# Kernel optimization log

Measured on AMD Instinct MI355X. Metric: run time of the kernel, lower is better.

## Reference

```python
import jax, jax.numpy as jnp
import numpy as np

CH = 256
CQK = CH // 8
B, H, W = 4, 64, 64


def setup_inputs() -> dict:
    key = jax.random.key(0)
    ks = jax.random.split(key, 8)
    s_qk = 1.0 / np.sqrt(CH)  # MSR init for 1x1 conv: std = 1/sqrt(fan_in)
    x = jax.random.normal(ks[0], (B, CH, H, W), dtype=jnp.float32)
    Wq = jax.random.normal(ks[1], (CQK, CH), dtype=jnp.float32) * s_qk
    bq = jnp.zeros((CQK,), dtype=jnp.float32)
    Wk = jax.random.normal(ks[2], (CQK, CH), dtype=jnp.float32) * s_qk
    bk = jnp.zeros((CQK,), dtype=jnp.float32)
    Wv = jax.random.normal(ks[3], (CH, CH), dtype=jnp.float32) * s_qk
    bv = jnp.zeros((CH,), dtype=jnp.float32)
    # NOTE: module inits gamma=0; use a nonzero value so the attention branch is active
    gamma = jnp.float32(0.5) * jnp.ones((1,), dtype=jnp.float32)
    return {"x": x, "Wq": Wq, "bq": bq, "Wk": Wk, "bk": bk, "Wv": Wv, "bv": bv, "gamma": gamma}


def reference(x, Wq, bq, Wk, bk, Wv, bv, gamma):
    b, c, h, w = x.shape
    n = h * w
    xf = x.reshape(b, c, n)  # [B, C, N]
    # 1x1 convs are per-pixel channel projections
    q = jnp.einsum('oc,bcn->bon', Wq, xf) + bq[:, None]  # [B, C/8, N]
    k = jnp.einsum('oc,bcn->bon', Wk, xf) + bk[:, None]  # [B, C/8, N]
    v = jnp.einsum('oc,bcn->bon', Wv, xf) + bv[:, None]  # [B, C, N]
    # scores[b, i, j] = q[:, i] . k[:, j]  (no scaling, as in source)
    att = jax.nn.softmax(jnp.einsum('bci,bcj->bij', q, k), axis=-1)  # [B, N, N]
    out = jnp.einsum('bcj,bij->bci', v, att).reshape(b, c, h, w)
    return x + gamma[0] * out
```

## Files before the change

kernel.cpp:

```cpp
#include <hip/hip_runtime.h>
#include <hip/hip_bf16.h>

typedef unsigned short u16;
typedef __attribute__((ext_vector_type(8))) __bf16 bf16x8;
typedef __attribute__((ext_vector_type(8))) short s16x8;
typedef __attribute__((ext_vector_type(8))) unsigned short u16x8;
typedef __attribute__((ext_vector_type(4))) float f32x4;
typedef __attribute__((ext_vector_type(16))) float f32x16;
typedef __attribute__((ext_vector_type(2))) unsigned int u32x2;

#define MFMA16(a, b, c) __builtin_amdgcn_mfma_f32_16x16x32_bf16((a), (b), (c), 0, 0, 0)
#define MFMA32(a, b, c) __builtin_amdgcn_mfma_f32_32x32x16_bf16((a), (b), (c), 0, 0, 0)

#define BN 4
#define CH 256
#define CQK 32
#define NPIX 4096

__device__ __forceinline__ u16 f2bf(float f) {
    __hip_bfloat16 h = __float2bfloat16(f);
    return *reinterpret_cast<u16*>(&h);
}

__device__ __forceinline__ unsigned pack2(float a, float b) {
    return (unsigned)f2bf(a) | ((unsigned)f2bf(b) << 16);
}

__device__ __forceinline__ float bf2f(u16 v) {
    return __uint_as_float(((unsigned)v) << 16);
}

__device__ __forceinline__ f32x16 zero16() {
    f32x16 z;
#pragma unroll
    for (int i = 0; i < 16; ++i) z[i] = 0.f;
    return z;
}

__device__ __forceinline__ int perm16(int k) {
    return (k & 3) | ((k & 4) << 1) | ((k & 8) >> 1);
}

__global__ void k_wcvt(const float* __restrict__ Wq, const float* __restrict__ Wk,
                       const float* __restrict__ Wv, u16* __restrict__ Wbf) {
    int idx = blockIdx.x * 256 + threadIdx.x;
    int o = idx >> 8, c = idx & 255;
    float v;
    if (o < 32) v = Wq[o * 256 + c];
    else if (o < 64) v = Wk[(o - 32) * 256 + c];
    else v = Wv[(o - 64) * 256 + c];
    Wbf[idx] = f2bf(v);
}

__launch_bounds__(256, 1)
__global__ void k_projf(const float* __restrict__ x, const u16* __restrict__ Wbf,
                        const float* __restrict__ bq, const float* __restrict__ bk,
                        const float* __restrict__ bv,
                        u16* __restrict__ qb, u16* __restrict__ kb, u16* __restrict__ vb) {
    int b = blockIdx.y, n0 = blockIdx.x * 64;
    int t = threadIdx.x, w = t >> 6, l = t & 63;
    int lr = l & 15, lg = l >> 4;

    __shared__ u16 xs[64][264];

    {
        int cs = t >> 4, ns = (t & 15) * 4;
#pragma unroll
        for (int p = 0; p < 16; ++p) {
            int c = p * 16 + cs;
            f32x4 v4 = *(const f32x4*)(x + ((size_t)(b * CH + c)) * NPIX + n0 + ns);
            xs[ns + 0][c] = f2bf(v4[0]);
            xs[ns + 1][c] = f2bf(v4[1]);
            xs[ns + 2][c] = f2bf(v4[2]);
            xs[ns + 3][c] = f2bf(v4[3]);
        }
    }
    __syncthreads();

    f32x4 acc[5][4];
#pragma unroll
    for (int s = 0; s < 5; ++s)
#pragma unroll
        for (int u = 0; u < 4; ++u) acc[s][u] = f32x4{0.f, 0.f, 0.f, 0.f};

#pragma unroll
    for (int kk = 0; kk < 8; ++kk) {
        int kof = kk * 32 + lg * 8;
        bf16x8 af[5], bfr[4];
#pragma unroll
        for (int s = 0; s < 5; ++s) {
            int o = w * 16 + s * 64 + lr;
            af[s] = *reinterpret_cast<const bf16x8*>(Wbf + (size_t)o * 256 + kof);
        }
#pragma unroll
        for (int u = 0; u < 4; ++u)
            bfr[u] = *reinterpret_cast<const bf16x8*>(&xs[u * 16 + lr][kof]);
#pragma unroll
        for (int s = 0; s < 5; ++s)
#pragma unroll
            for (int u = 0; u < 4; ++u) acc[s][u] = MFMA16(af[s], bfr[u], acc[s][u]);
    }

    int lrp = perm16(lr);
#pragma unroll
    for (int s = 0; s < 5; ++s) {
        int o0 = w * 16 + s * 64;
#pragma unroll
        for (int r = 0; r < 4; ++r) {
            int o = o0 + lg * 4 + r;
            float bias = (o < 32) ? bq[o] : (o < 64) ? bk[o - 32] : bv[o - 64];
#pragma unroll
            for (int u = 0; u < 4; ++u) {
                float val = acc[s][u][r] + bias;
                u16 h = f2bf(val);
                if (o < 32) qb[((size_t)b * NPIX + n0 + u * 16 + lr) * CQK + o] = h;
                else if (o < 64) kb[((size_t)b * NPIX + n0 + u * 16 + lr) * CQK + (o - 32)] = h;
                else vb[((size_t)(b * CH + (o - 64))) * NPIX + n0 + u * 16 + lrp] = h;
            }
        }
    }
}

template <int NCHUNK>
__launch_bounds__(256, 2)
__global__ void k_attn12(const u16* __restrict__ qb, const u16* __restrict__ kb,
                         const u16* __restrict__ vb, const float* __restrict__ x,
                         const float* __restrict__ gamma,
                         u16* __restrict__ pacc, float* __restrict__ plsum,
                         float* __restrict__ out) {
    constexpr int JCH = NPIX / NCHUNK;
    constexpr int NT = JCH / 32;
    int it = blockIdx.x, s = blockIdx.y, b = blockIdx.z;
    int t = threadIdx.x, w = t >> 6, l = t & 63;
    int lr = l & 31, hi = l >> 5;
    int i0 = it * 128;
    int j0 = s * JCH;

    __shared__ u16 vlds[2][256][40];
    __shared__ float lsl[128];

    const u16* qrow = qb + ((size_t)b * NPIX + i0 + w * 32 + lr) * CQK;
    bf16x8 qf0 = *(const bf16x8*)(qrow + hi * 8);
    bf16x8 qf1 = *(const bf16x8*)(qrow + 16 + hi * 8);

    const u16* kbase = kb + (size_t)b * NPIX * CQK;
    const u16* vbase = vb + (size_t)(b * CH) * NPIX;

    f32x16 acc[8];
#pragma unroll
    for (int ct = 0; ct < 8; ++ct) acc[ct] = zero16();
    float lsum_p = 0.f;

    int srow = t >> 2, swg = t & 3;

    bf16x8 vst[4];
#pragma unroll
    for (int m = 0; m < 4; ++m)
        vst[m] = *(const bf16x8*)(vbase + (size_t)(64 * m + srow) * NPIX + j0 + swg * 8);
#pragma unroll
    for (int m = 0; m < 4; ++m)
        *(bf16x8*)(&vlds[0][64 * m + srow][swg * 8]) = vst[m];
    __syncthreads();

    const u16* krow = kbase + (size_t)(j0 + lr) * CQK;
    bf16x8 kc0 = *(const bf16x8*)(krow + hi * 8);
    bf16x8 kc1 = *(const bf16x8*)(krow + 16 + hi * 8);

    for (int tt = 0; tt < NT; ++tt) {
        int cur = tt & 1;
        bool more = (tt + 1 < NT);
        int jn = j0 + (more ? (tt + 1) * 32 : 0);

        if (more) {
#pragma unroll
            for (int m = 0; m < 4; ++m)
                vst[m] = *(const bf16x8*)(vbase + (size_t)(64 * m + srow) * NPIX + jn + swg * 8);
        }
        const u16* krn = kbase + (size_t)(jn + lr) * CQK;
        bf16x8 kn0 = *(const bf16x8*)(krn + hi * 8);
        bf16x8 kn1 = *(const bf16x8*)(krn + 16 + hi * 8);

        f32x16 sf = MFMA32(kc0, qf0, zero16());
        sf = MFMA32(kc1, qf1, sf);

        float P[16];
#pragma unroll
        for (int r = 0; r < 16; ++r) {
            P[r] = __expf(sf[r] - 32.0f);
            lsum_p += P[r];
        }

        s16x8 w0, w1;
#pragma unroll
        for (int e = 0; e < 8; ++e) {
            w0[e] = (short)f2bf(P[e]);
            w1[e] = (short)f2bf(P[8 + e]);
        }
        bf16x8 pa0 = __builtin_bit_cast(bf16x8, w0);
        bf16x8 pa1 = __builtin_bit_cast(bf16x8, w1);

#pragma unroll
        for (int ct = 0; ct < 8; ++ct) {
            const u16* vr = &vlds[cur][ct * 32 + lr][hi * 8];
            bf16x8 vf0 = *(const bf16x8*)(vr);
            bf16x8 vf1 = *(const bf16x8*)(vr + 16);
            acc[ct] = MFMA32(pa0, vf0, acc[ct]);
            acc[ct] = MFMA32(pa1, vf1, acc[ct]);
        }
        kc0 = kn0; kc1 = kn1;

        __syncthreads();
        if (more) {
#pragma unroll
            for (int m = 0; m < 4; ++m)
                *(bf16x8*)(&vlds[cur ^ 1][64 * m + srow][swg * 8]) = vst[m];
        }
        __syncthreads();
    }

    lsum_p += __shfl_xor(lsum_p, 32);

    if constexpr (NCHUNK == 1) {
        float g = gamma[0];
        if (l < 32) lsl[w * 32 + l] = g / lsum_p;
        __syncthreads();
#pragma unroll
        for (int ct = 0; ct < 8; ++ct) {
            int c = ct * 32 + lr;
            const float* xp = x + ((size_t)(b * CH + c)) * NPIX + i0;
            float* op = out + ((size_t)(b * CH + c)) * NPIX + i0;
#pragma unroll
            for (int r = 0; r < 16; ++r) {
                int il = w * 32 + (r & 3) + 8 * (r >> 2) + 4 * hi;
                op[il] = xp[il] + acc[ct][r] * lsl[il];
            }
        }
    } else {
        size_t pbase = ((((size_t)s * BN + b) * 32 + it) * 256) * 128;
#pragma unroll
        for (int ct = 0; ct < 8; ++ct) {
            int c = ct * 32 + lr;
#pragma unroll
            for (int q = 0; q < 4; ++q) {
                int il0 = w * 32 + 8 * q + 4 * hi;
                u32x2 pr = {pack2(acc[ct][4 * q], acc[ct][4 * q + 1]),
                            pack2(acc[ct][4 * q + 2], acc[ct][4 * q + 3])};
                *(u32x2*)(pacc + pbase + (size_t)c * 128 + il0) = pr;
            }
        }
        if (l < 32)
            plsum[(((size_t)s * BN + b) * 32 + it) * 128 + w * 32 + l] = lsum_p;
    }
}

template <int NCHUNK>
__global__ void k_reduce(const u16* __restrict__ pacc, const float* __restrict__ plsum,
                         const float* __restrict__ x, const float* __restrict__ gamma,
                         float* __restrict__ out) {
    int cg = blockIdx.x, it = blockIdx.y, b = blockIdx.z;
    int t = threadIdx.x;
    int c0 = cg * 32;
    __shared__ float invl[128];

    if (t < 128) {
        float lt = 0.f;
#pragma unroll
        for (int s = 0; s < NCHUNK; ++s)
            lt += plsum[(((size_t)s * BN + b) * 32 + it) * 128 + t];
        invl[t] = gamma[0] / lt;
    }
    __syncthreads();

    const size_t chunk_stride = (size_t)BN * 32 * 256 * 128;
    size_t base = (((size_t)b * 32 + it) * 256 + c0) * 128;

#pragma unroll
    for (int k = 0; k < 2; ++k) {
        int v = k * 256 + t;
        int cl = v >> 4;
        int io = (v & 15) * 8;
        size_t off = base + (size_t)cl * 128 + io;
        f32x4 a0 = {0.f, 0.f, 0.f, 0.f}, a1 = a0;
#pragma unroll
        for (int s = 0; s < NCHUNK; ++s) {
            u16x8 p = *(const u16x8*)(pacc + (size_t)s * chunk_stride + off);
            a0[0] += bf2f(p[0]); a0[1] += bf2f(p[1]); a0[2] += bf2f(p[2]); a0[3] += bf2f(p[3]);
            a1[0] += bf2f(p[4]); a1[1] += bf2f(p[5]); a1[2] += bf2f(p[6]); a1[3] += bf2f(p[7]);
        }
        f32x4 i0v = *(const f32x4*)(&invl[io]);
        f32x4 i1v = *(const f32x4*)(&invl[io + 4]);
        size_t oi = ((size_t)(b * CH + c0 + cl)) * NPIX + it * 128 + io;
        f32x4 x0 = *(const f32x4*)(x + oi);
        f32x4 x1 = *(const f32x4*)(x + oi + 4);
        *(f32x4*)(out + oi) = x0 + a0 * i0v;
        *(f32x4*)(out + oi + 4) = x1 + a1 * i1v;
    }
}

extern "C" void kernel_launch(void* const* d_in, const int* in_sizes, int n_in,
                              void* d_out, int out_size, void* d_ws, size_t ws_size,
                              hipStream_t stream) {
    const float* x = (const float*)d_in[0];
    const float* Wq = (const float*)d_in[1];
    const float* bq = (const float*)d_in[2];
    const float* Wk = (const float*)d_in[3];
    const float* bk = (const float*)d_in[4];
    const float* Wv = (const float*)d_in[5];
    const float* bv = (const float*)d_in[6];
    const float* gamma = (const float*)d_in[7];
    float* out = (float*)d_out;

    char* ws = (char*)d_ws;
    u16* Wbf = (u16*)(ws + 8388608);
    u16* qb = (u16*)(ws + 8388608 + 163840);
    u16* kb = (u16*)(ws + 8388608 + 163840 + 1048576);
    u16* vb = (u16*)(ws + 8388608 + 163840 + 2097152);
    const size_t base_end = 8388608 + 163840 + 2097152 + 8388608;
    u16* pacc = (u16*)(ws + base_end);

    hipLaunchKernelGGL(k_wcvt, dim3(320), dim3(256), 0, stream, Wq, Wk, Wv, Wbf);
    hipLaunchKernelGGL(k_projf, dim3(64, 4), dim3(256), 0, stream,
                       x, Wbf, bq, bk, bv, qb, kb, vb);

    const size_t pacc4 = (size_t)4 * BN * NPIX * CH * 2;
    const size_t pls4 = (size_t)4 * BN * NPIX * 4;
    const size_t pacc2 = pacc4 / 2, pls2 = pls4 / 2;

    if (ws_size >= base_end + pacc4 + pls4) {
        float* plsum = (float*)(ws + base_end + pacc4);
        hipLaunchKernelGGL(k_attn12<4>, dim3(32, 4, 4), dim3(256), 0, stream,
                           qb, kb, vb, x, gamma, pacc, plsum, out);
        hipLaunchKernelGGL(k_reduce<4>, dim3(8, 32, 4), dim3(256), 0, stream,
                           pacc, plsum, x, gamma, out);
    } else if (ws_size >= base_end + pacc2 + pls2) {
        float* plsum = (float*)(ws + base_end + pacc2);
        hipLaunchKernelGGL(k_attn12<2>, dim3(32, 2, 4), dim3(256), 0, stream,
                           qb, kb, vb, x, gamma, pacc, plsum, out);
        hipLaunchKernelGGL(k_reduce<2>, dim3(8, 32, 4), dim3(256), 0, stream,
                           pacc, plsum, x, gamma, out);
    } else {
        hipLaunchKernelGGL(k_attn12<1>, dim3(32, 1, 4), dim3(256), 0, stream,
                           qb, kb, vb, x, gamma, pacc, (float*)pacc, out);
    }
}
```

Measured before the change: 85.05 us.

## Use four-slot V LDS ring and process two tiles per barrier

Replaces the double-buffered V tile with a four-slot LDS ring. The loop now handles two key tiles per iteration with a single __syncthreads, prefetching V two tiles ahead so that writing the next slots never conflicts with reads of the current ones. The aim is to cut barrier count and expose more memory/compute overlap. LDS usage doubles to about 80KB per block, which may hold occupancy below the two blocks per CU the launch bounds target.

```diff
diff --git a/kernel.cpp b/kernel.cpp
--- a/kernel.cpp
+++ b/kernel.cpp
@@ -123,7 +123,7 @@
 
 template <int NCHUNK>
 __launch_bounds__(256, 2)
-__global__ void k_attn12(const u16* __restrict__ qb, const u16* __restrict__ kb,
+__global__ void k_attn13(const u16* __restrict__ qb, const u16* __restrict__ kb,
                          const u16* __restrict__ vb, const float* __restrict__ x,
                          const float* __restrict__ gamma,
                          u16* __restrict__ pacc, float* __restrict__ plsum,
@@ -136,7 +136,7 @@
     int i0 = it * 128;
     int j0 = s * JCH;
 
-    __shared__ u16 vlds[2][256][40];
+    __shared__ u16 vlds[4][256][40];
     __shared__ float lsl[128];
 
     const u16* qrow = qb + ((size_t)b * NPIX + i0 + w * 32 + lr) * CQK;
@@ -153,43 +153,27 @@
 
     int srow = t >> 2, swg = t & 3;
 
-    bf16x8 vst[4];
-#pragma unroll
-    for (int m = 0; m < 4; ++m)
-        vst[m] = *(const bf16x8*)(vbase + (size_t)(64 * m + srow) * NPIX + j0 + swg * 8);
-#pragma unroll
-    for (int m = 0; m < 4; ++m)
-        *(bf16x8*)(&vlds[0][64 * m + srow][swg * 8]) = vst[m];
-    __syncthreads();
-
-    const u16* krow = kbase + (size_t)(j0 + lr) * CQK;
-    bf16x8 kc0 = *(const bf16x8*)(krow + hi * 8);
-    bf16x8 kc1 = *(const bf16x8*)(krow + 16 + hi * 8);
-
-    for (int tt = 0; tt < NT; ++tt) {
-        int cur = tt & 1;
-        bool more = (tt + 1 < NT);
-        int jn = j0 + (more ? (tt + 1) * 32 : 0);
-
-        if (more) {
-#pragma unroll
-            for (int m = 0; m < 4; ++m)
-                vst[m] = *(const bf16x8*)(vbase + (size_t)(64 * m + srow) * NPIX + jn + swg * 8);
-        }
-        const u16* krn = kbase + (size_t)(jn + lr) * CQK;
-        bf16x8 kn0 = *(const bf16x8*)(krn + hi * 8);
-        bf16x8 kn1 = *(const bf16x8*)(krn + 16 + hi * 8);
-
-        f32x16 sf = MFMA32(kc0, qf0, zero16());
-        sf = MFMA32(kc1, qf1, sf);
-
+    bf16x8 vstA[4], vstB[4];
+    auto vload = [&](bf16x8 (&vst)[4], int tt) {
+#pragma unroll
+        for (int m = 0; m < 4; ++m)
+            vst[m] = *(const bf16x8*)(vbase + (size_t)(64 * m + srow) * NPIX +
+                                      j0 + tt * 32 + swg * 8);
+    };
+    auto vwrite = [&](bf16x8 (&vst)[4], int slot) {
+#pragma unroll
+        for (int m = 0; m < 4; ++m)
+            *(bf16x8*)(&vlds[slot][64 * m + srow][swg * 8]) = vst[m];
+    };
+    auto tile = [&](int slot, bf16x8 k0, bf16x8 k1) {
+        f32x16 sf = MFMA32(k0, qf0, zero16());
+        sf = MFMA32(k1, qf1, sf);
         float P[16];
 #pragma unroll
         for (int r = 0; r < 16; ++r) {
             P[r] = __expf(sf[r] - 32.0f);
             lsum_p += P[r];
         }
-
         s16x8 w0, w1;
 #pragma unroll
         for (int e = 0; e < 8; ++e) {
@@ -198,23 +182,42 @@
         }
         bf16x8 pa0 = __builtin_bit_cast(bf16x8, w0);
         bf16x8 pa1 = __builtin_bit_cast(bf16x8, w1);
-
 #pragma unroll
         for (int ct = 0; ct < 8; ++ct) {
-            const u16* vr = &vlds[cur][ct * 32 + lr][hi * 8];
+            const u16* vr = &vlds[slot][ct * 32 + lr][hi * 8];
             bf16x8 vf0 = *(const bf16x8*)(vr);
             bf16x8 vf1 = *(const bf16x8*)(vr + 16);
             acc[ct] = MFMA32(pa0, vf0, acc[ct]);
             acc[ct] = MFMA32(pa1, vf1, acc[ct]);
         }
+    };
+    auto kload = [&](int tt, bf16x8& k0, bf16x8& k1) {
+        const u16* kr = kbase + (size_t)(j0 + tt * 32 + lr) * CQK;
+        k0 = *(const bf16x8*)(kr + hi * 8);
+        k1 = *(const bf16x8*)(kr + 16 + hi * 8);
+    };
+
+    vload(vstA, 0);
+    vwrite(vstA, 0);
+    vload(vstB, 1);
+    vwrite(vstB, 1);
+    __syncthreads();
+    bf16x8 kc0, kc1, kn0, kn1;
+    kload(0, kc0, kc1);
+
+    for (int tp = 0; tp < NT; tp += 2) {
+        bool m2 = (tp + 2 < NT);
+        bool m3 = (tp + 3 < NT);
+        if (m2) vload(vstA, tp + 2);
+        kload(tp + 1, kn0, kn1);
+        tile(tp & 3, kc0, kc1);
+        if (m2) vwrite(vstA, (tp + 2) & 3);
         kc0 = kn0; kc1 = kn1;
-
-        __syncthreads();
-        if (more) {
-#pragma unroll
-            for (int m = 0; m < 4; ++m)
-                *(bf16x8*)(&vlds[cur ^ 1][64 * m + srow][swg * 8]) = vst[m];
-        }
+        if (m3) vload(vstB, tp + 3);
+        if (m2) kload(tp + 2, kn0, kn1);
+        tile((tp + 1) & 3, kc0, kc1);
+        if (m3) vwrite(vstB, (tp + 3) & 3);
+        if (m2) { kc0 = kn0; kc1 = kn1; }
         __syncthreads();
     }
 
@@ -328,18 +331,18 @@
 
     if (ws_size >= base_end + pacc4 + pls4) {
         float* plsum = (float*)(ws + base_end + pacc4);
-        hipLaunchKernelGGL(k_attn12<4>, dim3(32, 4, 4), dim3(256), 0, stream,
+        hipLaunchKernelGGL(k_attn13<4>, dim3(32, 4, 4), dim3(256), 0, stream,
                            qb, kb, vb, x, gamma, pacc, plsum, out);
         hipLaunchKernelGGL(k_reduce<4>, dim3(8, 32, 4), dim3(256), 0, stream,
                            pacc, plsum, x, gamma, out);
     } else if (ws_size >= base_end + pacc2 + pls2) {
         float* plsum = (float*)(ws + base_end + pacc2);
-        hipLaunchKernelGGL(k_attn12<2>, dim3(32, 2, 4), dim3(256), 0, stream,
+        hipLaunchKernelGGL(k_attn13<2>, dim3(32, 2, 4), dim3(256), 0, stream,
                            qb, kb, vb, x, gamma, pacc, plsum, out);
         hipLaunchKernelGGL(k_reduce<2>, dim3(8, 32, 4), dim3(256), 0, stream,
                            pacc, plsum, x, gamma, out);
     } else {
-        hipLaunchKernelGGL(k_attn12<1>, dim3(32, 1, 4), dim3(256), 0, stream,
+        hipLaunchKernelGGL(k_attn13<1>, dim3(32, 1, 4), dim3(256), 0, stream,
                            qb, kb, vb, x, gamma, pacc, (float*)pacc, out);
     }
 }
```

Result: no change. 86.25 us (+1.4%).
